# Kernel tuning notes

Measured on AMD Instinct MI355X. Metric: run time of the kernel, lower is better.

Reference implementation:

```python
import jax, jax.numpy as jnp
import numpy as np
import math

MUL = 128
LS = [0, 1, 2]                                    # irreps_in = 128x0e + 128x1o + 128x2e
IN_DIM = MUL * sum(2 * l + 1 for l in LS)         # 1152
PATHS = [(0,0,0),(0,1,1),(0,2,2),(1,0,1),(1,1,0),(1,1,2),(1,2,1),(2,0,2),(2,1,1),(2,2,0),(2,2,2)]
LS_TP = [p[2] for p in PATHS]
NPATH = len(PATHS)                                # 11
NM_IN = len(LS) * MUL                             # 384 gate channels
NM_TP = NPATH * MUL                               # 1408 gate channels
N_NODES = 16384

# ---- real-basis Wigner 3j (e3nn convention) ----
def _su2_cg(j1, m1, j2, m2, j3, m3):
    if m3 != m1 + m2:
        return 0.0
    f = math.factorial
    vmin = max(-j1 + j2 + m3, -j1 + m1, 0)
    vmax = min(j2 + j3 + m1, j3 - j1 + j2, j3 + m3)
    c = math.sqrt((2 * j3 + 1) * f(j3 + j1 - j2) * f(j3 - j1 + j2) * f(j1 + j2 - j3)
                  * f(j3 + m3) * f(j3 - m3)
                  / (f(j1 + j2 + j3 + 1) * f(j1 - m1) * f(j1 + m1) * f(j2 - m2) * f(j2 + m2)))
    s = 0.0
    for v in range(vmin, vmax + 1):
        s += (-1) ** (v + j2 + m2) * f(j2 + j3 + m1 - v) * f(j1 - m1 + v) / (
            f(v) * f(j3 - j1 + j2 - v) * f(j3 + m3 - v) * f(v + j1 - j2 - m3))
    return c * s

def _q(l):
    q = np.zeros((2 * l + 1, 2 * l + 1), dtype=np.complex128)
    for m in range(-l, 0):
        q[l + m, l + abs(m)] = 1 / 2 ** 0.5
        q[l + m, l - abs(m)] = -1j / 2 ** 0.5
    q[l, l] = 1
    for m in range(1, l + 1):
        q[l + m, l + abs(m)] = (-1) ** m / 2 ** 0.5
        q[l + m, l - abs(m)] = 1j * (-1) ** m / 2 ** 0.5
    return (-1j) ** l * q

def _wigner_3j(l1, l2, l3):
    C = np.zeros((2 * l1 + 1, 2 * l2 + 1, 2 * l3 + 1))
    for m1 in range(-l1, l1 + 1):
        for m2 in range(-l2, l2 + 1):
            m3 = m1 + m2
            if abs(m3) <= l3:
                C[l1 + m1, l2 + m2, l3 + m3] = _su2_cg(l1, m1, l2, m2, l3, m3)
    C = C / math.sqrt(2 * l3 + 1)
    C = np.einsum('ij,kl,mn,ikm->jln', _q(l1), _q(l2), np.conj(_q(l3)), C.astype(np.complex128))
    return np.real(C).astype(np.float32)

W3J = {p: jnp.asarray(_wigner_3j(*p)) for p in set(PATHS)}

# ---- irrep block helpers (e3nn layout: [N, mul*(2l+1)] per group, concatenated) ----
def _split(x, ls):
    out, off = [], 0
    for l in ls:
        d = MUL * (2 * l + 1)
        out.append(x[:, off:off + d].reshape(x.shape[0], MUL, 2 * l + 1))
        off += d
    return out

def _merge(blocks):
    return jnp.concatenate([b.reshape(b.shape[0], -1) for b in blocks], axis=-1)

def _gate(x, ls, Wg, bg):
    # refine-Gate: per-channel invariants (scalar value / L2 norm) -> linear -> silu -> multiply
    blocks = _split(x, ls)
    invs = [b[:, :, 0] if l == 0 else jnp.sqrt(jnp.sum(b * b, axis=-1)) for b, l in zip(blocks, ls)]
    g = jax.nn.silu(jnp.concatenate(invs, axis=-1) @ Wg + bg)
    return _merge([b * g[:, i * MUL:(i + 1) * MUL, None] for i, b in enumerate(blocks)])

def _linear_sq(x, W0, W1, W2, b0):
    # o3.Linear(irreps_in, irreps_in, biases=True): block-diagonal per-l channel mixing
    b = _split(x, LS)
    inv = 1.0 / math.sqrt(MUL)
    o = [jnp.einsum('nui,uv->nvi', blk, W) * inv for blk, W in zip(b, (W0, W1, W2))]
    o[0] = o[0] + b0[None, :, None]
    return _merge(o)

def _tp_uuu(xl, xr, tp_w):
    # o3.TensorProduct 'uuu': channel-wise CG contraction, one learned weight per channel/path
    bl = _split(xl, LS)
    br = _split(xr, LS)
    outs = []
    for p, (l1, l2, lo) in enumerate(PATHS):
        o = math.sqrt(2 * lo + 1) * jnp.einsum('ijk,nui,nuj->nuk', W3J[(l1, l2, lo)], bl[l1], br[l2])
        outs.append(o * tp_w[p][None, :, None])
    return _merge(outs)

def _linear_p(x, Wp0, Wp1, Wp2):
    # o3.Linear(irreps_tp_out, irreps_hidden): mixes all tp groups of equal l into hidden group
    b = _split(x, LS_TP)
    outs = []
    for l, W in zip(LS, (Wp0, Wp1, Wp2)):
        xs = jnp.concatenate([blk for blk, lo in zip(b, LS_TP) if lo == l], axis=1)
        outs.append(jnp.einsum('nui,uv->nvi', xs, W) / math.sqrt(xs.shape[1]))
    return _merge(outs)

def setup_inputs() -> dict:
    key = jax.random.key(0)
    ks = jax.random.split(key, 16)
    f32 = jnp.float32
    rn = lambda k, shp: jax.random.normal(k, shp, dtype=f32)
    return {
        'x': rn(ks[0], (N_NODES, IN_DIM)),
        'fii_in': rn(ks[1], (N_NODES, IN_DIM)),
        'Wg_l': rn(ks[2], (NM_IN, NM_IN)) / math.sqrt(NM_IN),
        'bg_l': jnp.zeros((NM_IN,), f32),
        'Wl0': rn(ks[3], (MUL, MUL)), 'Wl1': rn(ks[4], (MUL, MUL)), 'Wl2': rn(ks[5], (MUL, MUL)),
        'bl0': jnp.zeros((MUL,), f32),
        'Wg_r': rn(ks[6], (NM_IN, NM_IN)) / math.sqrt(NM_IN),
        'bg_r': jnp.zeros((NM_IN,), f32),
        'Wr0': rn(ks[7], (MUL, MUL)), 'Wr1': rn(ks[8], (MUL, MUL)), 'Wr2': rn(ks[9], (MUL, MUL)),
        'br0': jnp.zeros((MUL,), f32),
        'tp_w': rn(ks[10], (NPATH, MUL)),
        'Wg_p': rn(ks[11], (NM_TP, NM_TP)) / math.sqrt(NM_TP),
        'bg_p': jnp.zeros((NM_TP,), f32),
        'Wp0': rn(ks[12], (3 * MUL, MUL)),
        'Wp1': rn(ks[13], (4 * MUL, MUL)),
        'Wp2': rn(ks[14], (4 * MUL, MUL)),
    }

def reference(x, fii_in, Wg_l, bg_l, Wl0, Wl1, Wl2, bl0, Wg_r, bg_r, Wr0, Wr1, Wr2, br0,
              tp_w, Wg_p, bg_p, Wp0, Wp1, Wp2):
    xl = _linear_sq(_gate(x, LS, Wg_l, bg_l), Wl0, Wl1, Wl2, bl0)
    xr = _linear_sq(_gate(x, LS, Wg_r, bg_r), Wr0, Wr1, Wr2, br0)
    xtp = _gate(_tp_uuu(xl, xr, tp_w), LS_TP, Wg_p, bg_p)
    return _linear_p(xtp, Wp0, Wp1, Wp2) + fii_in
```

## Files before the change

kernel.cpp:

```cpp
#include <hip/hip_runtime.h>
#include <hip/hip_bf16.h>
#include <cmath>
#include <complex>
#include <algorithm>

typedef __hip_bfloat16 bf16;
typedef __bf16 bf16x8 __attribute__((ext_vector_type(8)));
typedef float f32x4 __attribute__((ext_vector_type(4)));

#define NN 16384

constexpr int P_L1[11] = {0,0,0,1,1,1,1,2,2,2,2};
constexpr int P_L2[11] = {0,1,2,0,1,1,2,0,1,2,2};
constexpr int P_LO[11] = {0,1,2,1,0,2,1,2,1,0,2};
constexpr int P_OFF[11]= {0,1,10,35,44,53,98,143,168,213,238};
constexpr int P_G[11]  = {0,0,0,1,1,1,2,2,3,2,3};

struct W3JPack { float v[363]; };

__global__ __launch_bounds__(256) void invx_kernel(const float* __restrict__ x,
                                                   bf16* __restrict__ inv_x)
{
    int idx = blockIdx.x * 256 + threadIdx.x;
    int n = idx / 384, c = idx - n * 384;
    const float* p = x + (size_t)n * 1152;
    float v;
    if (c < 128) {
        v = p[c];
    } else if (c < 256) {
        const float* q = p + 128 + (c - 128) * 3;
        v = sqrtf(q[0]*q[0] + q[1]*q[1] + q[2]*q[2]);
    } else {
        const float* q = p + 512 + (c - 256) * 5;
        v = sqrtf(q[0]*q[0] + q[1]*q[1] + q[2]*q[2] + q[3]*q[3] + q[4]*q[4]);
    }
    inv_x[idx] = __float2bfloat16(v);
}

struct WPack {
    const float* W[12];
    bf16* Bt[12];
    int K[12];
    int Nn[12];
};

__global__ __launch_bounds__(256) void wconv_all(WPack wp)
{
    __shared__ float t[32][33];
    int z = blockIdx.z;
    int K = wp.K[z], Nn = wp.Nn[z];
    int bx = blockIdx.x * 32;
    int by = blockIdx.y * 32;
    if (bx >= Nn || by >= K) return;
    const float* W = wp.W[z];
    bf16* Bt = wp.Bt[z];
    int lx = threadIdx.x & 31, ly = threadIdx.x >> 5;
    #pragma unroll
    for (int yy = ly; yy < 32; yy += 8)
        t[yy][lx] = W[(size_t)(by + yy) * Nn + bx + lx];
    __syncthreads();
    #pragma unroll
    for (int yy = ly; yy < 32; yy += 8)
        Bt[(size_t)(bx + yy) * K + by + lx] = __float2bfloat16(t[lx][yy]);
}

__global__ __launch_bounds__(256) void gate_apply2(const float* __restrict__ x,
                                                   const bf16* __restrict__ gbuf,
                                                   bf16* __restrict__ xg_l,
                                                   bf16* __restrict__ xg_r, int Nc)
{
    int idx = blockIdx.x * 256 + threadIdx.x;
    int n = idx >> 7, u = idx & 127;
    const float* xrow = x + (size_t)n * 1152;
    const bf16* grow = gbuf + (size_t)n * 768;
    size_t O1 = (size_t)Nc * 128, O2 = (size_t)Nc * 512;
    float gl0 = __bfloat162float(grow[u]);
    float gl1 = __bfloat162float(grow[128 + u]);
    float gl2 = __bfloat162float(grow[256 + u]);
    float gr0 = __bfloat162float(grow[384 + u]);
    float gr1 = __bfloat162float(grow[512 + u]);
    float gr2 = __bfloat162float(grow[640 + u]);
    float x0 = xrow[u];
    xg_l[(size_t)n * 128 + u] = __float2bfloat16(x0 * gl0);
    xg_r[(size_t)n * 128 + u] = __float2bfloat16(x0 * gr0);
    #pragma unroll
    for (int i = 0; i < 3; ++i) {
        float xv = xrow[128 + u * 3 + i];
        xg_l[O1 + ((size_t)n * 3 + i) * 128 + u] = __float2bfloat16(xv * gl1);
        xg_r[O1 + ((size_t)n * 3 + i) * 128 + u] = __float2bfloat16(xv * gr1);
    }
    #pragma unroll
    for (int i = 0; i < 5; ++i) {
        float xv = xrow[512 + u * 5 + i];
        xg_l[O2 + ((size_t)n * 5 + i) * 128 + u] = __float2bfloat16(xv * gl2);
        xg_r[O2 + ((size_t)n * 5 + i) * 128 + u] = __float2bfloat16(xv * gr2);
    }
}

__device__ __forceinline__ void gemm_core(
    const bf16* __restrict__ A, const bf16* __restrict__ Bt, int K,
    int bm, int bn, int lane, int wid, char* AsB, char* BsB,
    const int* srow, const int* scol, f32x4 acc[4][4])
{
    const int wm = (wid >> 1) * 64;
    const int wn = (wid & 1) * 64;
    for (int k0 = 0; k0 < K; k0 += 64) {
        #pragma unroll
        for (int q = 0; q < 4; ++q) {
            const bf16* ga = A + (size_t)(bm + srow[q]) * K + k0 + scol[q];
            __builtin_amdgcn_global_load_lds(
                (const __attribute__((address_space(1))) void*)ga,
                (__attribute__((address_space(3))) void*)(AsB + wid * 4096 + q * 1024),
                16, 0, 0);
            const bf16* gb = Bt + (size_t)(bn + srow[q]) * K + k0 + scol[q];
            __builtin_amdgcn_global_load_lds(
                (const __attribute__((address_space(1))) void*)gb,
                (__attribute__((address_space(3))) void*)(BsB + wid * 4096 + q * 1024),
                16, 0, 0);
        }
        asm volatile("s_waitcnt vmcnt(0)" ::: "memory");
        __syncthreads();
        #pragma unroll
        for (int kh = 0; kh < 2; ++kh) {
            bf16x8 av[4], bv[4];
            #pragma unroll
            for (int m = 0; m < 4; ++m) {
                int row = wm + m * 16 + (lane & 15);
                int off = row * 128 + kh * 64 + ((lane >> 4) << 4);
                off ^= (row & 7) << 4;
                av[m] = *reinterpret_cast<const bf16x8*>(AsB + off);
            }
            #pragma unroll
            for (int n = 0; n < 4; ++n) {
                int row = wn + n * 16 + (lane & 15);
                int off = row * 128 + kh * 64 + ((lane >> 4) << 4);
                off ^= (row & 7) << 4;
                bv[n] = *reinterpret_cast<const bf16x8*>(BsB + off);
            }
            #pragma unroll
            for (int m = 0; m < 4; ++m)
                #pragma unroll
                for (int n = 0; n < 4; ++n)
                    acc[m][n] = __builtin_amdgcn_mfma_f32_16x16x32_bf16(av[m], bv[n], acc[m][n], 0, 0, 0);
        }
        __syncthreads();
    }
}

__device__ __forceinline__ void stage_coords(int lane, int wid, int* srow, int* scol)
{
    #pragma unroll
    for (int q = 0; q < 4; ++q) {
        int d = wid * 4096 + q * 1024 + lane * 16;
        int row = d >> 7;
        int colb = (d & 127) ^ ((row & 7) << 4);
        srow[q] = row;
        scol[q] = colb >> 1;
    }
}

__global__ __launch_bounds__(256) void mgemm(
    const bf16* __restrict__ A, const bf16* __restrict__ Bt,
    const float* __restrict__ bias, const float* __restrict__ bias2, int split,
    bf16* __restrict__ C, int Nn, int K)
{
    __shared__ __align__(16) char Lds[32768];
    char* AsB = Lds;
    char* BsB = Lds + 16384;
    const int tid = threadIdx.x;
    const int lane = tid & 63;
    const int wid = tid >> 6;

    int nwg = gridDim.x * gridDim.y;
    int orig = blockIdx.y * gridDim.x + blockIdx.x;
    int q8 = nwg >> 3, r8 = nwg & 7;
    int xcd = orig & 7, pos = orig >> 3;
    int t = (xcd < r8 ? xcd * (q8 + 1) : r8 * (q8 + 1) + (xcd - r8) * q8) + pos;
    const int bm = (t / gridDim.x) * 128;
    const int bn = (t % gridDim.x) * 128;

    int srow[4], scol[4];
    stage_coords(lane, wid, srow, scol);

    f32x4 acc[4][4];
    #pragma unroll
    for (int m = 0; m < 4; ++m)
        #pragma unroll
        for (int n = 0; n < 4; ++n)
            acc[m][n] = (f32x4){0.f, 0.f, 0.f, 0.f};

    gemm_core(A, Bt, K, bm, bn, lane, wid, AsB, BsB, srow, scol, acc);

    const int wm = (wid >> 1) * 64;
    const int wn = (wid & 1) * 64;
    #pragma unroll
    for (int m = 0; m < 4; ++m) {
        int row0 = bm + wm + m * 16 + ((lane >> 4) << 2);
        #pragma unroll
        for (int n = 0; n < 4; ++n) {
            int col = bn + wn + n * 16 + (lane & 15);
            float b = (col < split) ? bias[col] : bias2[col - split];
            #pragma unroll
            for (int r = 0; r < 4; ++r) {
                float z = acc[m][n][r] + b;
                z = z / (1.f + __expf(-z));
                C[(size_t)(row0 + r) * Nn + col] = __float2bfloat16(z);
            }
        }
    }
}

struct SegPack {
    const bf16* A[6];
    const bf16* Bt[6];
    const float* bias[6];
    bf16* out[6];
    float scale[6];
    int K[6];
    int segEnd[6];
    int ooff[6];
    int span[6];
};

template<int EPI>
__global__ __launch_bounds__(256) void mgemm_seg(
    SegPack sp, const float* __restrict__ fii, float* __restrict__ outf)
{
    __shared__ __align__(16) char Lds[32768];
    char* AsB = Lds;
    char* BsB = Lds + 16384;
    const int tid = threadIdx.x;
    const int lane = tid & 63;
    const int wid = tid >> 6;

    int by = blockIdx.y;
    int s = 0;
    while (by >= sp.segEnd[s]) ++s;
    int prev = s ? sp.segEnd[s - 1] : 0;
    const int bm = (by - prev) * 128;
    const bf16* A = sp.A[s];
    const bf16* Bt = sp.Bt[s];
    const int K = sp.K[s];
    const float scale = sp.scale[s];

    int srow[4], scol[4];
    stage_coords(lane, wid, srow, scol);

    f32x4 acc[4][4];
    #pragma unroll
    for (int m = 0; m < 4; ++m)
        #pragma unroll
        for (int n = 0; n < 4; ++n)
            acc[m][n] = (f32x4){0.f, 0.f, 0.f, 0.f};

    gemm_core(A, Bt, K, bm, 0, lane, wid, AsB, BsB, srow, scol, acc);

    const int wm = (wid >> 1) * 64;
    const int wn = (wid & 1) * 64;
    if (EPI == 1) {
        const float* bias = sp.bias[s];
        bf16* out = sp.out[s];
        #pragma unroll
        for (int m = 0; m < 4; ++m) {
            int row0 = bm + wm + m * 16 + ((lane >> 4) << 2);
            #pragma unroll
            for (int n = 0; n < 4; ++n) {
                int col = wn + n * 16 + (lane & 15);
                float b = bias ? bias[col] : 0.f;
                #pragma unroll
                for (int r = 0; r < 4; ++r) {
                    float z = acc[m][n][r] * scale + b;
                    out[(size_t)(row0 + r) * 128 + col] = __float2bfloat16(z);
                }
            }
        }
    } else {
        const int span = sp.span[s];
        const int ooff = sp.ooff[s];
        #pragma unroll
        for (int m = 0; m < 4; ++m) {
            int row0 = bm + wm + m * 16 + ((lane >> 4) << 2);
            #pragma unroll
            for (int n = 0; n < 4; ++n) {
                int col = wn + n * 16 + (lane & 15);
                #pragma unroll
                for (int r = 0; r < 4; ++r) {
                    int row = row0 + r;
                    int nn = row / span, i = row - nn * span;
                    size_t oidx = (size_t)nn * 1152 + ooff + (size_t)col * span + i;
                    outf[oidx] = acc[m][n][r] * scale + fii[oidx];
                }
            }
        }
    }
}

__global__ __launch_bounds__(256) void tp_kernel(
    const bf16* __restrict__ xl, const bf16* __restrict__ xr,
    const float* __restrict__ tp_w, const bf16* __restrict__ gp,
    bf16* __restrict__ inv_tp,
    bf16* __restrict__ tpg0, bf16* __restrict__ tpg1, bf16* __restrict__ tpg2,
    W3JPack w3j, int phase, int Nc)
{
    int idx = blockIdx.x * 256 + threadIdx.x;
    int n = idx >> 7, u = idx & 127;
    const size_t O1 = (size_t)Nc * 128, O2 = (size_t)Nc * 512;
    float XL[3][5], XR[3][5];
    XL[0][0] = __bfloat162float(xl[(size_t)n * 128 + u]);
    XR[0][0] = __bfloat162float(xr[(size_t)n * 128 + u]);
    #pragma unroll
    for (int i = 0; i < 3; ++i) {
        XL[1][i] = __bfloat162float(xl[O1 + ((size_t)n * 3 + i) * 128 + u]);
        XR[1][i] = __bfloat162float(xr[O1 + ((size_t)n * 3 + i) * 128 + u]);
    }
    #pragma unroll
    for (int i = 0; i < 5; ++i) {
        XL[2][i] = __bfloat162float(xl[O2 + ((size_t)n * 5 + i) * 128 + u]);
        XR[2][i] = __bfloat162float(xr[O2 + ((size_t)n * 5 + i) * 128 + u]);
    }
    const float SQF[3] = {1.f, 1.7320508075688772f, 2.2360679774997896f};
    #pragma unroll
    for (int p = 0; p < 11; ++p) {
        const int l1 = P_L1[p], l2 = P_L2[p], lo = P_LO[p];
        const int d1 = 2*l1+1, d2 = 2*l2+1, dd = 2*lo+1;
        const float* W = &w3j.v[P_OFF[p]];
        float tw = tp_w[p * 128 + u] * SQF[lo];
        float o[5];
        #pragma unroll
        for (int k = 0; k < dd; ++k) {
            float a = 0.f;
            #pragma unroll
            for (int i = 0; i < d1; ++i)
                #pragma unroll
                for (int jj = 0; jj < d2; ++jj)
                    a += W[(i * d2 + jj) * dd + k] * XL[l1][i] * XR[l2][jj];
            o[k] = a * tw;
        }
        if (phase == 0) {
            float iv;
            if (lo == 0) iv = o[0];
            else {
                float s = 0.f;
                #pragma unroll
                for (int k = 0; k < dd; ++k) s += o[k] * o[k];
                iv = sqrtf(s);
            }
            inv_tp[(size_t)n * 1408 + p * 128 + u] = __float2bfloat16(iv);
        } else {
            float g = __bfloat162float(gp[(size_t)n * 1408 + p * 128 + u]);
            int gg = P_G[p];
            if (lo == 0) {
                tpg0[(size_t)n * 384 + gg * 128 + u] = __float2bfloat16(o[0] * g);
            } else if (lo == 1) {
                #pragma unroll
                for (int k = 0; k < 3; ++k)
                    tpg1[((size_t)n * 3 + k) * 512 + gg * 128 + u] = __float2bfloat16(o[k] * g);
            } else {
                #pragma unroll
                for (int k = 0; k < 5; ++k)
                    tpg2[((size_t)n * 5 + k) * 512 + gg * 128 + u] = __float2bfloat16(o[k] * g);
            }
        }
    }
}

static double factd(int n) {
    static const double F[10] = {1,1,2,6,24,120,720,5040,40320,362880};
    return F[n];
}

static double su2_cg(int j1,int m1,int j2,int m2,int j3,int m3){
    if (m3 != m1 + m2) return 0.0;
    int vmin = std::max(std::max(-j1 + j2 + m3, -j1 + m1), 0);
    int vmax = std::min(std::min(j2 + j3 + m1, j3 - j1 + j2), j3 + m3);
    if (vmax < vmin) return 0.0;
    double c = std::sqrt((2*j3+1) * factd(j3+j1-j2) * factd(j3-j1+j2) * factd(j1+j2-j3)
               * factd(j3+m3) * factd(j3-m3)
               / (factd(j1+j2+j3+1) * factd(j1-m1) * factd(j1+m1) * factd(j2-m2) * factd(j2+m2)));
    double s = 0.0;
    for (int v = vmin; v <= vmax; ++v) {
        double sg = ((v + j2 + m2) & 1) ? -1.0 : 1.0;
        s += sg * factd(j2+j3+m1-v) * factd(j1-m1+v)
             / (factd(v) * factd(j3-j1+j2-v) * factd(j3+m3-v) * factd(v+j1-j2-m3));
    }
    return c * s;
}

typedef std::complex<double> cd;

static void q_matrix(int l, cd* q) {
    int d = 2*l+1;
    for (int i = 0; i < d*d; ++i) q[i] = cd(0,0);
    const double is2 = 1.0 / std::sqrt(2.0);
    for (int m = -l; m < 0; ++m) {
        q[(l+m)*d + (l-m)] = cd(is2, 0);
        q[(l+m)*d + (l+m)] = cd(0, -is2);
    }
    q[l*d + l] = cd(1,0);
    for (int m = 1; m <= l; ++m) {
        double sg = (m & 1) ? -1.0 : 1.0;
        q[(l+m)*d + (l+m)] = cd(sg*is2, 0);
        q[(l+m)*d + (l-m)] = cd(0, sg*is2);
    }
    cd f = (l==0) ? cd(1,0) : (l==1) ? cd(0,-1) : cd(-1,0);
    for (int i = 0; i < d*d; ++i) q[i] *= f;
}

static void compute_w3j(float* out) {
    for (int p = 0; p < 11; ++p) {
        int l1 = P_L1[p], l2 = P_L2[p], l3 = P_LO[p];
        int d1 = 2*l1+1, d2 = 2*l2+1, d3 = 2*l3+1;
        cd q1[25], q2[25], q3[25];
        q_matrix(l1, q1); q_matrix(l2, q2); q_matrix(l3, q3);
        double nrm = std::sqrt((double)d3);
        for (int a = 0; a < d1; ++a)
        for (int b = 0; b < d2; ++b)
        for (int c = 0; c < d3; ++c) {
            cd s(0,0);
            for (int i = 0; i < d1; ++i)
            for (int k = 0; k < d2; ++k)
            for (int m = 0; m < d3; ++m) {
                double cg = su2_cg(l1, i-l1, l2, k-l2, l3, m-l3);
                if (cg == 0.0) continue;
                s += q1[i*d1 + a] * q2[k*d2 + b] * std::conj(q3[m*d3 + c]) * cg;
            }
            out[P_OFF[p] + (a*d2 + b)*d3 + c] = (float)(s.real() / nrm);
        }
    }
}

extern "C" void kernel_launch(void* const* d_in, const int* in_sizes, int n_in,
                              void* d_out, int out_size, void* d_ws, size_t ws_size,
                              hipStream_t stream)
{
    (void)in_sizes; (void)n_in; (void)out_size;
    const float* x    = (const float*)d_in[0];
    const float* fii  = (const float*)d_in[1];
    const float* Wg_l = (const float*)d_in[2];
    const float* bg_l = (const float*)d_in[3];
    const float* Wl0  = (const float*)d_in[4];
    const float* Wl1  = (const float*)d_in[5];
    const float* Wl2  = (const float*)d_in[6];
    const float* bl0  = (const float*)d_in[7];
    const float* Wg_r = (const float*)d_in[8];
    const float* bg_r = (const float*)d_in[9];
    const float* Wr0  = (const float*)d_in[10];
    const float* Wr1  = (const float*)d_in[11];
    const float* Wr2  = (const float*)d_in[12];
    const float* br0  = (const float*)d_in[13];
    const float* tp_w = (const float*)d_in[14];
    const float* Wg_p = (const float*)d_in[15];
    const float* bg_p = (const float*)d_in[16];
    const float* Wp0  = (const float*)d_in[17];
    const float* Wp1  = (const float*)d_in[18];
    const float* Wp2  = (const float*)d_in[19];
    float* out = (float*)d_out;

    W3JPack w3j;
    compute_w3j(w3j.v);

    auto al = [](size_t b) { return (b + 255) & ~(size_t)255; };
    char* base = (char*)d_ws;
    size_t woff = 0;
    auto walloc = [&](size_t elems) { void* p = base + woff; woff += al(elems * 2); return (bf16*)p; };
    bf16* tWg   = walloc((size_t)768 * 384);
    bf16* tWl0  = walloc(128 * 128);
    bf16* tWl1  = walloc(128 * 128);
    bf16* tWl2  = walloc(128 * 128);
    bf16* tWr0  = walloc(128 * 128);
    bf16* tWr1  = walloc(128 * 128);
    bf16* tWr2  = walloc(128 * 128);
    bf16* tWg_p = walloc((size_t)1408 * 1408);
    bf16* tWp0  = walloc(128 * 384);
    bf16* tWp1  = walloc(128 * 512);
    bf16* tWp2  = walloc(128 * 512);
    const size_t wtotal = woff;

    int c = 1; size_t Nc;
    for (;; c *= 2) {
        Nc = NN / c;
        size_t tot = wtotal + 2 * al(Nc * 2304) + al(Nc * 11776);
        if (tot <= ws_size || c >= 32) break;
    }
    char* cb = base + wtotal;
    bf16* xl = (bf16*)cb;  cb += al(Nc * 2304);
    bf16* xr = (bf16*)cb;  cb += al(Nc * 2304);
    char* R3 = cb;
    bf16* inv_x = (bf16*)R3;
    bf16* gbuf  = (bf16*)(R3 + Nc * 768);
    bf16* xg_l  = (bf16*)(R3 + Nc * 2304);
    bf16* xg_r  = (bf16*)(R3 + Nc * 4608);
    bf16* inv_tp = (bf16*)R3;
    bf16* tpg0   = (bf16*)R3;
    bf16* tpg1   = (bf16*)(R3 + Nc * 768);
    bf16* tpg2   = (bf16*)(R3 + Nc * 3840);
    bf16* gp     = (bf16*)(R3 + Nc * 8960);

    const float s128 = 0.08838834764831845f;
    const float s384 = 0.05103103630798287f;
    const float s512 = 0.044194173824159216f;
    dim3 blk(256);

    WPack wp;
    wp.W[0] = Wg_l; wp.Bt[0] = tWg;             wp.K[0] = 384;  wp.Nn[0] = 384;
    wp.W[1] = Wg_r; wp.Bt[1] = tWg + 384*384;   wp.K[1] = 384;  wp.Nn[1] = 384;
    wp.W[2] = Wl0;  wp.Bt[2] = tWl0;            wp.K[2] = 128;  wp.Nn[2] = 128;
    wp.W[3] = Wl1;  wp.Bt[3] = tWl1;            wp.K[3] = 128;  wp.Nn[3] = 128;
    wp.W[4] = Wl2;  wp.Bt[4] = tWl2;            wp.K[4] = 128;  wp.Nn[4] = 128;
    wp.W[5] = Wr0;  wp.Bt[5] = tWr0;            wp.K[5] = 128;  wp.Nn[5] = 128;
    wp.W[6] = Wr1;  wp.Bt[6] = tWr1;            wp.K[6] = 128;  wp.Nn[6] = 128;
    wp.W[7] = Wr2;  wp.Bt[7] = tWr2;            wp.K[7] = 128;  wp.Nn[7] = 128;
    wp.W[8] = Wg_p; wp.Bt[8] = tWg_p;           wp.K[8] = 1408; wp.Nn[8] = 1408;
    wp.W[9] = Wp0;  wp.Bt[9] = tWp0;            wp.K[9] = 384;  wp.Nn[9] = 128;
    wp.W[10]= Wp1;  wp.Bt[10]= tWp1;            wp.K[10]= 512;  wp.Nn[10]= 128;
    wp.W[11]= Wp2;  wp.Bt[11]= tWp2;            wp.K[11]= 512;  wp.Nn[11]= 128;
    wconv_all<<<dim3(44, 44, 12), blk, 0, stream>>>(wp);

    const int gy = (int)(Nc / 128);
    for (int ch = 0; ch < c; ++ch) {
        const float* xc = x   + (size_t)ch * Nc * 1152;
        const float* fc = fii + (size_t)ch * Nc * 1152;
        float*       oc = out + (size_t)ch * Nc * 1152;

        invx_kernel<<<dim3((int)(Nc * 384 / 256)), blk, 0, stream>>>(xc, inv_x);

        mgemm<<<dim3(6, gy), blk, 0, stream>>>(inv_x, tWg, bg_l, bg_r, 384,
                                               gbuf, 768, 384);

        gate_apply2<<<dim3((int)(Nc / 2)), blk, 0, stream>>>(xc, gbuf, xg_l, xg_r, (int)Nc);

        {
            SegPack sp{};
            const bf16* As[6]  = {xg_l, xg_l + Nc*128, xg_l + Nc*512,
                                  xg_r, xg_r + Nc*128, xg_r + Nc*512};
            const bf16* Bs[6]  = {tWl0, tWl1, tWl2, tWr0, tWr1, tWr2};
            const float* bi[6] = {bl0, nullptr, nullptr, br0, nullptr, nullptr};
            bf16* os[6]        = {xl, xl + Nc*128, xl + Nc*512,
                                  xr, xr + Nc*128, xr + Nc*512};
            int rows[6] = {gy, 3*gy, 5*gy, gy, 3*gy, 5*gy};
            int acc_r = 0;
            for (int s = 0; s < 6; ++s) {
                sp.A[s] = As[s]; sp.Bt[s] = Bs[s]; sp.bias[s] = bi[s]; sp.out[s] = os[s];
                sp.scale[s] = s128; sp.K[s] = 128;
                acc_r += rows[s]; sp.segEnd[s] = acc_r;
                sp.ooff[s] = 0; sp.span[s] = 1;
            }
            mgemm_seg<1><<<dim3(1, 18*gy), blk, 0, stream>>>(sp, nullptr, nullptr);
        }

        tp_kernel<<<dim3((int)(Nc / 2)), blk, 0, stream>>>(xl, xr, tp_w, gp, inv_tp,
            tpg0, tpg1, tpg2, w3j, 0, (int)Nc);

        mgemm<<<dim3(11, gy), blk, 0, stream>>>(inv_tp, tWg_p, bg_p, nullptr, 1408,
                                                gp, 1408, 1408);

        tp_kernel<<<dim3((int)(Nc / 2)), blk, 0, stream>>>(xl, xr, tp_w, gp, inv_tp,
            tpg0, tpg1, tpg2, w3j, 1, (int)Nc);

        {
            SegPack sp{};
            sp.A[0] = tpg0; sp.Bt[0] = tWp0; sp.K[0] = 384; sp.scale[0] = s384;
            sp.segEnd[0] = gy;      sp.ooff[0] = 0;   sp.span[0] = 1;
            sp.A[1] = tpg1; sp.Bt[1] = tWp1; sp.K[1] = 512; sp.scale[1] = s512;
            sp.segEnd[1] = 4*gy;    sp.ooff[1] = 128; sp.span[1] = 3;
            sp.A[2] = tpg2; sp.Bt[2] = tWp2; sp.K[2] = 512; sp.scale[2] = s512;
            sp.segEnd[2] = 9*gy;    sp.ooff[2] = 512; sp.span[2] = 5;
            for (int s = 3; s < 6; ++s) sp.segEnd[s] = 9*gy + 1 + s;
            mgemm_seg<2><<<dim3(1, 9*gy), blk, 0, stream>>>(sp, fc, oc);
        }
    }
}
```

Before: 605.6 us.

## Double-buffer LDS tiles in GEMM core to overlap global loads with MFMA

Splits the K loop into a staging lambda and a main loop that prefetches the next 64-wide K tile into a second LDS buffer while MFMAs consume the current one. It waits with a partial vmcnt so only the older loads must finish. It also raises wave priority around the MFMA block. LDS per block doubles to 64 KB, which may reduce occupancy. The raw s_barrier calls replace __syncthreads and may leave LDS reads unfenced.

```diff
diff --git a/kernel.cpp b/kernel.cpp
--- a/kernel.cpp
+++ b/kernel.cpp
@@ -104,22 +104,37 @@
 {
     const int wm = (wid >> 1) * 64;
     const int wn = (wid & 1) * 64;
-    for (int k0 = 0; k0 < K; k0 += 64) {
+    const int nsteps = K >> 6;
+
+    auto stage = [&](int buf, int t) {
+        int k0 = t << 6;
         #pragma unroll
         for (int q = 0; q < 4; ++q) {
             const bf16* ga = A + (size_t)(bm + srow[q]) * K + k0 + scol[q];
             __builtin_amdgcn_global_load_lds(
                 (const __attribute__((address_space(1))) void*)ga,
-                (__attribute__((address_space(3))) void*)(AsB + wid * 4096 + q * 1024),
+                (__attribute__((address_space(3))) void*)(AsB + buf * 16384 + wid * 4096 + q * 1024),
                 16, 0, 0);
             const bf16* gb = Bt + (size_t)(bn + srow[q]) * K + k0 + scol[q];
             __builtin_amdgcn_global_load_lds(
                 (const __attribute__((address_space(1))) void*)gb,
-                (__attribute__((address_space(3))) void*)(BsB + wid * 4096 + q * 1024),
+                (__attribute__((address_space(3))) void*)(BsB + buf * 16384 + wid * 4096 + q * 1024),
                 16, 0, 0);
         }
-        asm volatile("s_waitcnt vmcnt(0)" ::: "memory");
-        __syncthreads();
+    };
+
+    stage(0, 0);
+    int cur = 0;
+    for (int t = 0; t < nsteps; ++t) {
+        if (t + 1 < nsteps) {
+            stage(cur ^ 1, t + 1);
+            asm volatile("s_waitcnt vmcnt(8)" ::: "memory");
+        } else {
+            asm volatile("s_waitcnt vmcnt(0)" ::: "memory");
+        }
+        __builtin_amdgcn_s_barrier();
+        char* Ab = AsB + cur * 16384;
+        char* Bb = BsB + cur * 16384;
         #pragma unroll
         for (int kh = 0; kh < 2; ++kh) {
             bf16x8 av[4], bv[4];
@@ -128,22 +143,25 @@
                 int row = wm + m * 16 + (lane & 15);
                 int off = row * 128 + kh * 64 + ((lane >> 4) << 4);
                 off ^= (row & 7) << 4;
-                av[m] = *reinterpret_cast<const bf16x8*>(AsB + off);
+                av[m] = *reinterpret_cast<const bf16x8*>(Ab + off);
             }
             #pragma unroll
             for (int n = 0; n < 4; ++n) {
                 int row = wn + n * 16 + (lane & 15);
                 int off = row * 128 + kh * 64 + ((lane >> 4) << 4);
                 off ^= (row & 7) << 4;
-                bv[n] = *reinterpret_cast<const bf16x8*>(BsB + off);
-            }
+                bv[n] = *reinterpret_cast<const bf16x8*>(Bb + off);
+            }
+            __builtin_amdgcn_s_setprio(1);
             #pragma unroll
             for (int m = 0; m < 4; ++m)
                 #pragma unroll
                 for (int n = 0; n < 4; ++n)
                     acc[m][n] = __builtin_amdgcn_mfma_f32_16x16x32_bf16(av[m], bv[n], acc[m][n], 0, 0, 0);
-        }
-        __syncthreads();
+            __builtin_amdgcn_s_setprio(0);
+        }
+        __builtin_amdgcn_s_barrier();
+        cur ^= 1;
     }
 }
 
@@ -164,9 +182,9 @@
     const float* __restrict__ bias, const float* __restrict__ bias2, int split,
     bf16* __restrict__ C, int Nn, int K)
 {
-    __shared__ __align__(16) char Lds[32768];
+    __shared__ __align__(16) char Lds[65536];
     char* AsB = Lds;
-    char* BsB = Lds + 16384;
+    char* BsB = Lds + 32768;
     const int tid = threadIdx.x;
     const int lane = tid & 63;
     const int wid = tid >> 6;
@@ -226,9 +244,9 @@
 __global__ __launch_bounds__(256) void mgemm_seg(
     SegPack sp, const float* __restrict__ fii, float* __restrict__ outf)
 {
-    __shared__ __align__(16) char Lds[32768];
+    __shared__ __align__(16) char Lds[65536];
     char* AsB = Lds;
-    char* BsB = Lds + 16384;
+    char* BsB = Lds + 32768;
     const int tid = threadIdx.x;
     const int lane = tid & 63;
     const int wid = tid >> 6;
```

Result: faster. 559.5 us (-7.6%).
